# Kernel optimization log

Measured on AMD Instinct MI355X. Metric: run time of the kernel, lower is better.

## Reference

```python
import jax, jax.numpy as jnp
import numpy as np
from jax import lax

B, T, D_IN, HID, C = 256, 1024, 39, 128, 41
H = HID // 2  # per-direction hidden = 64
G = 4 * H    # gate dim = 256


def _lstm_dir(x, w_ih, w_hh, b, reverse):
    # x: [B,T,Din]; w_ih: [4H,Din]; w_hh: [4H,H]; b: [4H] (b_ih+b_hh fused)
    gx = jnp.einsum('btd,gd->btg', x, w_ih) + b          # [B,T,4H]
    gx_t = jnp.swapaxes(gx, 0, 1)                        # [T,B,4H]
    h0 = jnp.zeros((x.shape[0], H), x.dtype)
    c0 = jnp.zeros((x.shape[0], H), x.dtype)

    def step(carry, g_t):
        h, c = carry
        gates = g_t + h @ w_hh.T
        i, f, g, o = jnp.split(gates, 4, axis=-1)        # torch gate order i,f,g,o
        i = jax.nn.sigmoid(i); f = jax.nn.sigmoid(f)
        g = jnp.tanh(g);       o = jax.nn.sigmoid(o)
        c = f * c + i * g
        h = o * jnp.tanh(c)
        return (h, c), h

    _, hs = lax.scan(step, (h0, c0), gx_t, reverse=reverse)
    return jnp.swapaxes(hs, 0, 1)                        # [B,T,H]


def _bilstm(x, w_ih_l0, w_hh_l0, b_l0, w_ih_r, w_hh_r, b_r):
    # layer 0: input dim 39
    hf = _lstm_dir(x, w_ih_l0[0], w_hh_l0[0], b_l0[0], False)
    hb = _lstm_dir(x, w_ih_l0[1], w_hh_l0[1], b_l0[1], True)
    h = jnp.concatenate([hf, hb], axis=-1)               # [B,T,128]
    # layers 1,2: input dim 128 (dropout is identity in eval mode)
    for l in range(2):
        hf = _lstm_dir(h, w_ih_r[l, 0], w_hh_r[l, 0], b_r[l, 0], False)
        hb = _lstm_dir(h, w_ih_r[l, 1], w_hh_r[l, 1], b_r[l, 1], True)
        h = jnp.concatenate([hf, hb], axis=-1)
    return h


def _viterbi(emissions, start, end, trans):
    # emissions [B,T,C] -> best tag path [B,T]
    e = jnp.swapaxes(emissions, 0, 1)                    # [T,B,C]
    score0 = start + e[0]                                # [B,C]

    def step(score, e_t):
        cand = score[:, :, None] + trans[None]           # [B,C_prev,C_next]
        best = jnp.max(cand, axis=1) + e_t
        idx = jnp.argmax(cand, axis=1)                   # [B,C] backpointers
        return best, idx

    final, hist = lax.scan(step, score0, e[1:])          # hist [T-1,B,C]
    final = final + end
    last = jnp.argmax(final, axis=-1)                    # [B]

    def back(tag, idx_t):
        prev = jnp.take_along_axis(idx_t, tag[:, None], axis=1)[:, 0]
        return prev, prev

    _, tags_rev = lax.scan(back, last, hist, reverse=True)  # [T-1,B] in time order
    tags = jnp.concatenate([tags_rev, last[None]], axis=0)  # [T,B]
    return jnp.swapaxes(tags, 0, 1).astype(jnp.int32)       # [B,T]


def setup_inputs() -> dict:
    key = jax.random.key(0)
    ks = jax.random.split(key, 12)
    s = 0.1
    return {
        'x':        jax.random.normal(ks[0], (B, T, D_IN), jnp.float32),
        'w_ih_l0':  jax.random.normal(ks[1], (2, G, D_IN), jnp.float32) * s,
        'w_hh_l0':  jax.random.normal(ks[2], (2, G, H), jnp.float32) * s,
        'b_l0':     jax.random.normal(ks[3], (2, G), jnp.float32) * s,
        'w_ih_r':   jax.random.normal(ks[4], (2, 2, G, HID), jnp.float32) * s,
        'w_hh_r':   jax.random.normal(ks[5], (2, 2, G, H), jnp.float32) * s,
        'b_r':      jax.random.normal(ks[6], (2, 2, G), jnp.float32) * s,
        'lin_w':    jax.random.normal(ks[7], (C, HID), jnp.float32) * s,
        'lin_b':    jax.random.normal(ks[8], (C,), jnp.float32) * s,
        'crf_start': jax.random.normal(ks[9], (C,), jnp.float32) * s,
        'crf_end':  jax.random.normal(ks[10], (C,), jnp.float32) * s,
        'crf_trans': jax.random.normal(ks[11], (C, C), jnp.float32) * s,
    }


def reference(x, w_ih_l0, w_hh_l0, b_l0, w_ih_r, w_hh_r, b_r,
              lin_w, lin_b, crf_start, crf_end, crf_trans):
    feats = _bilstm(x, w_ih_l0, w_hh_l0, b_l0, w_ih_r, w_hh_r, b_r)  # [B,T,128]
    emissions = jnp.einsum('bth,ch->btc', feats, lin_w) + lin_b      # [B,T,41]
    return _viterbi(emissions, crf_start, crf_end, crf_trans)        # [B,T] int32
```

## Files before the change

kernel.cpp:

```cpp
#include <hip/hip_runtime.h>

#define TT 1024
#define BB 256
#define CC 41

__device__ __forceinline__ float sigf(float x) {
    float t = __builtin_amdgcn_exp2f(-1.4426950408889634f * x);
    return __builtin_amdgcn_rcpf(1.0f + t);
}
__device__ __forceinline__ float tanhf_fast(float x) {
    float t = __builtin_amdgcn_exp2f(2.8853900817779268f * x);
    return fmaf(-2.0f, __builtin_amdgcn_rcpf(t + 1.0f), 1.0f);
}
__device__ __forceinline__ float lane_bcast(float v, int k) {
    return __uint_as_float(__builtin_amdgcn_readlane(__float_as_uint(v), k));
}

template <int PS, bool SPLIT>
__global__ __launch_bounds__(256, 2) void gemm_phase(
    const float* __restrict__ A0, int sA0,
    const float* __restrict__ A1, int sA1,
    const float* __restrict__ W,
    const float* __restrict__ bias,
    float* __restrict__ slab, size_t slabDirStride,
    int K, int phase, int dir_base)
{
    __shared__ float As[32][132];
    __shared__ float Bs[32][132];
    const int tid = threadIdx.x;
    const int bx = blockIdx.x;
    const int n0 = blockIdx.y * 128;
    const int dir = dir_base + blockIdx.z;
    const int tb = dir ? (TT - 1 - phase * PS) : (phase * PS);
    const float* Wd = W + (size_t)dir * 256 * K;
    const float* bd = bias + dir * 256;
    float* slabD = slab + slabDirStride * blockIdx.z;

    const int ty = tid >> 4, tx = tid & 15;
    float acc[8][8];
#pragma unroll
    for (int i = 0; i < 8; ++i)
#pragma unroll
        for (int j = 0; j < 8; ++j) acc[i][j] = 0.f;

    for (int k0 = 0; k0 < K; k0 += 32) {
        const int kc = (K - k0 < 32) ? (K - k0) : 32;
        if (SPLIT) {
            const bool hi = (k0 >= 64);
            const float* base = hi ? A1 : A0;
            const int str = hi ? sA1 : sA0;
            const int ko = k0 - (hi ? 64 : 0);
#pragma unroll
            for (int q = 0; q < 4; ++q) {
                const int lin = tid + q * 256;
                const int m = lin >> 3, c4 = lin & 7;
                const int r = bx * (128 / PS) + m / PS;
                const int s = m % PS;
                const int t = dir ? (tb - s) : (tb + s);
                const float4 v =
                    *(const float4*)(base + (size_t)(r * TT + t) * str + ko + c4 * 4);
                As[c4 * 4 + 0][m] = v.x; As[c4 * 4 + 1][m] = v.y;
                As[c4 * 4 + 2][m] = v.z; As[c4 * 4 + 3][m] = v.w;
            }
        } else if (kc == 32) {
#pragma unroll
            for (int q = 0; q < 16; ++q) {
                const int lin = tid + q * 256;
                const int m = lin >> 5, cc = lin & 31;
                const int r = bx * (128 / PS) + m / PS;
                const int s = m % PS;
                const int t = dir ? (tb - s) : (tb + s);
                As[cc][m] = A0[(size_t)(r * TT + t) * sA0 + k0 + cc];
            }
        } else {
            for (int lin = tid; lin < 128 * kc; lin += 256) {
                const int m = lin / kc, cc = lin - m * kc;
                const int r = bx * (128 / PS) + m / PS;
                const int s = m % PS;
                const int t = dir ? (tb - s) : (tb + s);
                As[cc][m] = A0[(size_t)(r * TT + t) * sA0 + k0 + cc];
            }
        }
        if (kc == 32) {
#pragma unroll
            for (int q = 0; q < 16; ++q) {
                const int lin = tid + q * 256;
                const int n = lin >> 5, cc = lin & 31;
                Bs[cc][n] = Wd[(size_t)(n0 + n) * K + k0 + cc];
            }
        } else {
            for (int lin = tid; lin < 128 * kc; lin += 256) {
                const int n = lin / kc, cc = lin - n * kc;
                Bs[cc][n] = Wd[(size_t)(n0 + n) * K + k0 + cc];
            }
        }
        __syncthreads();

        for (int kk = 0; kk < kc; ++kk) {
            float a[8], b[8];
            *(float4*)&a[0] = *(const float4*)&As[kk][ty * 4];
            *(float4*)&a[4] = *(const float4*)&As[kk][64 + ty * 4];
            *(float4*)&b[0] = *(const float4*)&Bs[kk][tx * 4];
            *(float4*)&b[4] = *(const float4*)&Bs[kk][64 + tx * 4];
#pragma unroll
            for (int i = 0; i < 8; ++i)
#pragma unroll
                for (int j = 0; j < 8; ++j)
                    acc[i][j] = fmaf(a[i], b[j], acc[i][j]);
        }
        __syncthreads();
    }

    float b0[4], b1[4];
#pragma unroll
    for (int j = 0; j < 4; ++j) {
        b0[j] = bd[n0 + tx * 4 + j];
        b1[j] = bd[n0 + 64 + tx * 4 + j];
    }
#pragma unroll
    for (int i = 0; i < 8; ++i) {
        const int m = (i < 4) ? (ty * 4 + i) : (64 + ty * 4 + i - 4);
        const int r = bx * (128 / PS) + m / PS;
        const int s = m % PS;
        float* so_ = slabD + ((size_t)r * PS + s) * 256;
        float4 v0, v1;
        v0.x = acc[i][0] + b0[0]; v0.y = acc[i][1] + b0[1];
        v0.z = acc[i][2] + b0[2]; v0.w = acc[i][3] + b0[3];
        v1.x = acc[i][4] + b1[0]; v1.y = acc[i][5] + b1[1];
        v1.z = acc[i][6] + b1[2]; v1.w = acc[i][7] + b1[3];
        *(float4*)&so_[n0 + tx * 4] = v0;
        *(float4*)&so_[n0 + 64 + tx * 4] = v1;
    }
}

template <int PS>
__global__ __launch_bounds__(64, 1) void recur_phase(
    const float* __restrict__ slab, size_t slabDirStride,
    const float* __restrict__ w_hh,
    float* __restrict__ outF, int strF,
    float* __restrict__ outB, int strB,
    float* __restrict__ state,
    int phase, int dir_base)
{
    const int r = blockIdx.x;
    const int dir = dir_base + blockIdx.y;
    const int j = threadIdx.x;

    float wi[64], wf[64], wg[64], wo[64];
    const float* wb = w_hh + (size_t)dir * 256 * 64;
#pragma unroll
    for (int q = 0; q < 16; ++q) {
        float4 v;
        v = *(const float4*)&wb[(size_t)j * 64 + q * 4];
        wi[q * 4] = v.x; wi[q * 4 + 1] = v.y; wi[q * 4 + 2] = v.z; wi[q * 4 + 3] = v.w;
        v = *(const float4*)&wb[(size_t)(64 + j) * 64 + q * 4];
        wf[q * 4] = v.x; wf[q * 4 + 1] = v.y; wf[q * 4 + 2] = v.z; wf[q * 4 + 3] = v.w;
        v = *(const float4*)&wb[(size_t)(128 + j) * 64 + q * 4];
        wg[q * 4] = v.x; wg[q * 4 + 1] = v.y; wg[q * 4 + 2] = v.z; wg[q * 4 + 3] = v.w;
        v = *(const float4*)&wb[(size_t)(192 + j) * 64 + q * 4];
        wo[q * 4] = v.x; wo[q * 4 + 1] = v.y; wo[q * 4 + 2] = v.z; wo[q * 4 + 3] = v.w;
    }

    float* stp = state + ((size_t)dir * 256 + r) * 128 + j;
    float h = 0.f, c = 0.f;
    if (phase != 0) { h = stp[0]; c = stp[64]; }

    const float* gx = slab + slabDirStride * blockIdx.y + (size_t)r * PS * 256 + j;
    const int tb = dir ? (TT - 1 - phase * PS) : (phase * PS);
    float* out = dir ? outB : outF;
    const int str = dir ? strB : strF;
    const ptrdiff_t hstep = dir ? -(ptrdiff_t)str : (ptrdiff_t)str;
    float* hp = out + (size_t)(r * TT + tb) * str + j;

    float pg[4][4];
#pragma unroll
    for (int p = 0; p < 4; ++p) {
        const float* g0 = gx + (size_t)p * 256;
        pg[p][0] = g0[0]; pg[p][1] = g0[64]; pg[p][2] = g0[128]; pg[p][3] = g0[192];
    }

#pragma unroll 1
    for (int s4 = 0; s4 < PS; s4 += 4) {
#pragma unroll
        for (int u = 0; u < 4; ++u) {
            const int s = s4 + u;
            float ai = pg[u][0], af = pg[u][1], ag = pg[u][2], ao = pg[u][3];
            if (s + 4 < PS) {
                const float* gn = gx + (size_t)(s + 4) * 256;
                pg[u][0] = gn[0]; pg[u][1] = gn[64];
                pg[u][2] = gn[128]; pg[u][3] = gn[192];
            }
#pragma unroll
            for (int k = 0; k < 64; ++k) {
                const float hk = lane_bcast(h, k);
                ai = fmaf(hk, wi[k], ai);
                af = fmaf(hk, wf[k], af);
                ag = fmaf(hk, wg[k], ag);
                ao = fmaf(hk, wo[k], ao);
            }
            const float iv = sigf(ai), fv = sigf(af);
            const float gv = tanhf_fast(ag), ov = sigf(ao);
            c = fmaf(fv, c, iv * gv);
            h = ov * tanhf_fast(c);
            hp[0] = h;
            hp += hstep;
        }
    }
    stp[0] = h; stp[64] = c;
}

__global__ __launch_bounds__(256, 2) void emis_kernel(
    const float* __restrict__ hA,
    const float* __restrict__ hB,
    const float* __restrict__ lw, const float* __restrict__ lb,
    float* __restrict__ eout)
{
    __shared__ float sf[64 * 132];
    __shared__ float swt[41 * 132];
    const int tid = threadIdx.x;
    const size_t bt0 = (size_t)blockIdx.x * 64;

#pragma unroll
    for (int q = 0; q < 4; ++q) {
        const int idx = tid + q * 256;
        const int row = idx >> 4, c4 = idx & 15;
        *(float4*)&sf[row * 132 + c4 * 4] =
            *(const float4*)&hA[(bt0 + row) * 128 + c4 * 4];
    }
#pragma unroll
    for (int q = 0; q < 4; ++q) {
        const int idx = tid + q * 256;
        const int row = idx >> 4, c4 = idx & 15;
        *(float4*)&sf[row * 132 + 64 + c4 * 4] =
            *(const float4*)&hB[(bt0 + row) * 64 + c4 * 4];
    }
    for (int idx = tid; idx < 41 * 32; idx += 256) {
        const int row = idx >> 5, cc = idx & 31;
        *(float4*)&swt[row * 132 + cc * 4] = ((const float4*)lw)[idx];
    }
    __syncthreads();

    const int btg = tid >> 4;
    const int cg = tid & 15;
    const int c0 = cg * 3;
    float acc[4][3];
#pragma unroll
    for (int i = 0; i < 4; ++i)
#pragma unroll
        for (int j = 0; j < 3; ++j) acc[i][j] = 0.f;

    for (int k = 0; k < 128; k += 4) {
        float4 fv[4], wv[3];
#pragma unroll
        for (int i = 0; i < 4; ++i) fv[i] = *(const float4*)&sf[(btg * 4 + i) * 132 + k];
#pragma unroll
        for (int j = 0; j < 3; ++j) {
            const int c = (c0 + j < CC) ? (c0 + j) : (CC - 1);
            wv[j] = *(const float4*)&swt[c * 132 + k];
        }
#pragma unroll
        for (int i = 0; i < 4; ++i)
#pragma unroll
            for (int j = 0; j < 3; ++j) {
                acc[i][j] = fmaf(fv[i].x, wv[j].x, acc[i][j]);
                acc[i][j] = fmaf(fv[i].y, wv[j].y, acc[i][j]);
                acc[i][j] = fmaf(fv[i].z, wv[j].z, acc[i][j]);
                acc[i][j] = fmaf(fv[i].w, wv[j].w, acc[i][j]);
            }
    }
    __syncthreads();
    float* so = sf;
#pragma unroll
    for (int i = 0; i < 4; ++i)
#pragma unroll
        for (int j = 0; j < 3; ++j) {
            const int c = c0 + j;
            if (c < CC) so[(btg * 4 + i) * CC + c] = acc[i][j] + lb[c];
        }
    __syncthreads();
    for (int q = tid; q < 64 * CC; q += 256) {
        const int row = q / CC, col = q - row * CC;
        eout[(bt0 + row) * 128 + col] = so[q];
    }
}

__global__ __launch_bounds__(128, 1) void viterbi_kernel(
    const float* __restrict__ h0,
    const float* __restrict__ st, const float* __restrict__ en,
    const float* __restrict__ tr, int* __restrict__ out)
{
    const int b = blockIdx.x;
    const int tid = threadIdx.x;
    const int ci = tid >> 1;
    const int ph = tid & 1;
    const bool valid = (ci < CC);
    const int c = valid ? ci : (CC - 1);
    const int pbase = ph ? 20 : 0;

    __shared__ unsigned char bp[TT][CC];
    __shared__ float scp[2][CC];

    float trc[21];
#pragma unroll
    for (int i = 0; i < 21; ++i) trc[i] = tr[(pbase + i) * CC + c];

    const float* eb = h0 + (size_t)b * TT * 128 + 64;
    const float NEG = -3.0e38f;

    if (valid && ph == 0) scp[0][c] = st[c] + eb[c];
    __syncthreads();

#pragma unroll 1
    for (int t = 1; t < TT; ++t) {
        const int cur = (t - 1) & 1, nxt = t & 1;
        const float ecur = eb[(size_t)t * 128 + c];

        float best = NEG;
        int bi = 0;
#pragma unroll
        for (int i = 0; i < 21; ++i) {
            const float v = scp[cur][pbase + i] + trc[i];
            if (v > best) { best = v; bi = pbase + i; }
        }
        const float ob = __shfl_xor(best, 1, 64);
        const int oi = __shfl_xor(bi, 1, 64);
        float wv; int wi_;
        if (ph == 0) {
            const bool hw = (ob > best);
            wv = hw ? ob : best;
            wi_ = hw ? oi : bi;
        } else {
            const bool lw = !(best > ob);
            wv = lw ? ob : best;
            wi_ = lw ? oi : bi;
        }
        if (valid && ph == 0) {
            bp[t][c] = (unsigned char)wi_;
            scp[nxt][c] = wv + ecur;
        }
        __syncthreads();
    }

    const int lane = tid & 63;
    float fin = (tid < CC) ? scp[(TT - 1) & 1][lane] + en[lane] : NEG;
    int idx = lane;
#pragma unroll
    for (int off = 32; off; off >>= 1) {
        const float v2 = __shfl_down(fin, off, 64);
        const int i2 = __shfl_down(idx, off, 64);
        if (v2 > fin || (v2 == fin && i2 < idx)) { fin = v2; idx = i2; }
    }
    int tag = __shfl(idx, 0, 64);
    if (tid == 0) {
        int* ob = out + (size_t)b * TT;
        ob[TT - 1] = tag;
        for (int t = TT - 1; t >= 1; --t) {
            tag = bp[t][tag];
            ob[t - 1] = tag;
        }
    }
}

extern "C" void kernel_launch(void* const* d_in, const int* in_sizes, int n_in,
                              void* d_out, int out_size, void* d_ws, size_t ws_size,
                              hipStream_t stream) {
    const float* x       = (const float*)d_in[0];
    const float* w_ih_l0 = (const float*)d_in[1];
    const float* w_hh_l0 = (const float*)d_in[2];
    const float* b_l0    = (const float*)d_in[3];
    const float* w_ih_r  = (const float*)d_in[4];
    const float* w_hh_r  = (const float*)d_in[5];
    const float* b_r     = (const float*)d_in[6];
    const float* lin_w   = (const float*)d_in[7];
    const float* lin_b   = (const float*)d_in[8];
    const float* crf_s   = (const float*)d_in[9];
    const float* crf_e   = (const float*)d_in[10];
    const float* crf_t   = (const float*)d_in[11];
    int* out = (int*)d_out;

    float* H0    = (float*)d_ws;
    float* F     = H0 + (size_t)BB * TT * 128;
    float* slab  = F + (size_t)BB * TT * 64;
    float* state = slab + (size_t)BB * 128 * 256;

    const size_t SLAB0 = (size_t)BB * 64 * 256;
    for (int ph = 0; ph < 16; ++ph) {
        gemm_phase<64, false><<<dim3(128, 2, 2), 256, 0, stream>>>(
            x, 39, nullptr, 0, w_ih_l0, b_l0, slab, SLAB0, 39, ph, 0);
        recur_phase<64><<<dim3(256, 2), 64, 0, stream>>>(
            slab, SLAB0, w_hh_l0, H0, 128, H0 + 64, 128, state, ph, 0);
    }

    for (int l = 0; l < 2; ++l) {
        const float* W    = w_ih_r + (size_t)l * 512 * 128;
        const float* bias = b_r + (size_t)l * 512;
        const float* whh  = w_hh_r + (size_t)l * 512 * 64;
        const float* A0   = (l == 0) ? H0 : F;
        const int    s0   = (l == 0) ? 128 : 64;
        const float* A1   = H0 + 64;  const int s1 = 128;
        float* oF = (l == 0) ? F : H0;        const int sF = (l == 0) ? 64 : 128;
        float* oB = (l == 0) ? H0 + 64 : F;   const int sB = (l == 0) ? 128 : 64;
        for (int d = 0; d < 2; ++d) {
            for (int ph = 0; ph < 8; ++ph) {
                gemm_phase<128, true><<<dim3(256, 2, 1), 256, 0, stream>>>(
                    A0, s0, A1, s1, W, bias, slab, 0, 128, ph, d);
                recur_phase<128><<<dim3(256, 1), 64, 0, stream>>>(
                    slab, 0, whh, oF, sF, oB, sB, state, ph, d);
            }
        }
    }

    emis_kernel<<<BB * TT / 64, 256, 0, stream>>>(H0, F, lin_w, lin_b, H0 + 64);
    viterbi_kernel<<<BB, 128, 0, stream>>>(H0, crf_s, crf_e, crf_t, out);
}
```

Baseline: 6.931 ms.

## Use packed FMA with LDS-broadcast h in recurrence, prefetching GEMM and Viterbi

The recurrence kernel now stores h in shared memory and reads it back as float2 pairs. This replaces 64 per-step readlane broadcasts with half as many packed v2f FMAs, split into two partial sums. A dedicated recurrent-layer GEMM prefetches the next K chunk into registers while the current chunk is computed. Layer 0 moves to 128-step phases, which halves its launch count. Viterbi gains a tree-shaped argmax and an 8-step emission prefetch. The h exchange through LDS relies on single-wavefront ordering without a barrier, which the compiler could in principle reorder.

```diff
diff --git a/kernel.cpp b/kernel.cpp
--- a/kernel.cpp
+++ b/kernel.cpp
@@ -4,6 +4,8 @@
 #define BB 256
 #define CC 41
 
+typedef float v2f __attribute__((ext_vector_type(2)));
+
 __device__ __forceinline__ float sigf(float x) {
     float t = __builtin_amdgcn_exp2f(-1.4426950408889634f * x);
     return __builtin_amdgcn_rcpf(1.0f + t);
@@ -12,25 +14,20 @@
     float t = __builtin_amdgcn_exp2f(2.8853900817779268f * x);
     return fmaf(-2.0f, __builtin_amdgcn_rcpf(t + 1.0f), 1.0f);
 }
-__device__ __forceinline__ float lane_bcast(float v, int k) {
-    return __uint_as_float(__builtin_amdgcn_readlane(__float_as_uint(v), k));
-}
-
-template <int PS, bool SPLIT>
-__global__ __launch_bounds__(256, 2) void gemm_phase(
+
+template <int PS>
+__global__ __launch_bounds__(256, 2) void gemm_l0(
     const float* __restrict__ A0, int sA0,
-    const float* __restrict__ A1, int sA1,
-    const float* __restrict__ W,
-    const float* __restrict__ bias,
+    const float* __restrict__ W, const float* __restrict__ bias,
     float* __restrict__ slab, size_t slabDirStride,
-    int K, int phase, int dir_base)
+    int K, int phase)
 {
     __shared__ float As[32][132];
     __shared__ float Bs[32][132];
     const int tid = threadIdx.x;
     const int bx = blockIdx.x;
     const int n0 = blockIdx.y * 128;
-    const int dir = dir_base + blockIdx.z;
+    const int dir = blockIdx.z;
     const int tb = dir ? (TT - 1 - phase * PS) : (phase * PS);
     const float* Wd = W + (size_t)dir * 256 * K;
     const float* bd = bias + dir * 256;
@@ -45,24 +42,7 @@
 
     for (int k0 = 0; k0 < K; k0 += 32) {
         const int kc = (K - k0 < 32) ? (K - k0) : 32;
-        if (SPLIT) {
-            const bool hi = (k0 >= 64);
-            const float* base = hi ? A1 : A0;
-            const int str = hi ? sA1 : sA0;
-            const int ko = k0 - (hi ? 64 : 0);
-#pragma unroll
-            for (int q = 0; q < 4; ++q) {
-                const int lin = tid + q * 256;
-                const int m = lin >> 3, c4 = lin & 7;
-                const int r = bx * (128 / PS) + m / PS;
-                const int s = m % PS;
-                const int t = dir ? (tb - s) : (tb + s);
-                const float4 v =
-                    *(const float4*)(base + (size_t)(r * TT + t) * str + ko + c4 * 4);
-                As[c4 * 4 + 0][m] = v.x; As[c4 * 4 + 1][m] = v.y;
-                As[c4 * 4 + 2][m] = v.z; As[c4 * 4 + 3][m] = v.w;
-            }
-        } else if (kc == 32) {
+        if (kc == 32) {
 #pragma unroll
             for (int q = 0; q < 16; ++q) {
                 const int lin = tid + q * 256;
@@ -72,6 +52,12 @@
                 const int t = dir ? (tb - s) : (tb + s);
                 As[cc][m] = A0[(size_t)(r * TT + t) * sA0 + k0 + cc];
             }
+#pragma unroll
+            for (int q = 0; q < 16; ++q) {
+                const int lin = tid + q * 256;
+                const int n = lin >> 5, cc = lin & 31;
+                Bs[cc][n] = Wd[(size_t)(n0 + n) * K + k0 + cc];
+            }
         } else {
             for (int lin = tid; lin < 128 * kc; lin += 256) {
                 const int m = lin / kc, cc = lin - m * kc;
@@ -80,22 +66,12 @@
                 const int t = dir ? (tb - s) : (tb + s);
                 As[cc][m] = A0[(size_t)(r * TT + t) * sA0 + k0 + cc];
             }
-        }
-        if (kc == 32) {
-#pragma unroll
-            for (int q = 0; q < 16; ++q) {
-                const int lin = tid + q * 256;
-                const int n = lin >> 5, cc = lin & 31;
-                Bs[cc][n] = Wd[(size_t)(n0 + n) * K + k0 + cc];
-            }
-        } else {
             for (int lin = tid; lin < 128 * kc; lin += 256) {
                 const int n = lin / kc, cc = lin - n * kc;
                 Bs[cc][n] = Wd[(size_t)(n0 + n) * K + k0 + cc];
             }
         }
         __syncthreads();
-
         for (int kk = 0; kk < kc; ++kk) {
             float a[8], b[8];
             *(float4*)&a[0] = *(const float4*)&As[kk][ty * 4];
@@ -133,6 +109,111 @@
     }
 }
 
+__global__ __launch_bounds__(256, 2) void gemm_rec(
+    const float* __restrict__ A0, int sA0,
+    const float* __restrict__ A1, int sA1,
+    const float* __restrict__ W,
+    const float* __restrict__ bias,
+    float* __restrict__ slab,
+    int phase, int dir)
+{
+    __shared__ float As[32][132];
+    __shared__ float Bs[32][132];
+    const int tid = threadIdx.x;
+    const int bx = blockIdx.x;
+    const int n0 = blockIdx.y * 128;
+    const int tb = dir ? (TT - 1 - phase * 128) : (phase * 128);
+    const float* Wd = W + (size_t)dir * 256 * 128;
+    const float* bd = bias + dir * 256;
+
+    const int ty = tid >> 4, tx = tid & 15;
+    const int c4 = tid & 7;
+    const int mb = tid >> 3;
+
+    int rowoff[4];
+#pragma unroll
+    for (int q = 0; q < 4; ++q) {
+        const int s = mb + q * 32;
+        const int t = dir ? (tb - s) : (tb + s);
+        rowoff[q] = bx * TT + t;
+    }
+
+    float acc[8][8];
+#pragma unroll
+    for (int i = 0; i < 8; ++i)
+#pragma unroll
+        for (int j = 0; j < 8; ++j) acc[i][j] = 0.f;
+
+    float4 ra[4], rb[4];
+#pragma unroll
+    for (int q = 0; q < 4; ++q)
+        ra[q] = *(const float4*)&A0[(size_t)rowoff[q] * sA0 + c4 * 4];
+#pragma unroll
+    for (int q = 0; q < 4; ++q)
+        rb[q] = *(const float4*)&Wd[(size_t)(n0 + mb + q * 32) * 128 + c4 * 4];
+
+#pragma unroll
+    for (int ch = 0; ch < 4; ++ch) {
+#pragma unroll
+        for (int q = 0; q < 4; ++q) {
+            const int m = mb + q * 32;
+            As[c4 * 4 + 0][m] = ra[q].x; As[c4 * 4 + 1][m] = ra[q].y;
+            As[c4 * 4 + 2][m] = ra[q].z; As[c4 * 4 + 3][m] = ra[q].w;
+        }
+#pragma unroll
+        for (int q = 0; q < 4; ++q) {
+            const int n = mb + q * 32;
+            Bs[c4 * 4 + 0][n] = rb[q].x; Bs[c4 * 4 + 1][n] = rb[q].y;
+            Bs[c4 * 4 + 2][n] = rb[q].z; Bs[c4 * 4 + 3][n] = rb[q].w;
+        }
+        if (ch < 3) {
+            const int kn = (ch + 1) * 32;
+            const float* base = (kn >= 64) ? A1 : A0;
+            const int str = (kn >= 64) ? sA1 : sA0;
+            const int ko = kn - ((kn >= 64) ? 64 : 0);
+#pragma unroll
+            for (int q = 0; q < 4; ++q)
+                ra[q] = *(const float4*)&base[(size_t)rowoff[q] * str + ko + c4 * 4];
+#pragma unroll
+            for (int q = 0; q < 4; ++q)
+                rb[q] = *(const float4*)&Wd[(size_t)(n0 + mb + q * 32) * 128 + kn + c4 * 4];
+        }
+        __syncthreads();
+        for (int kk = 0; kk < 32; ++kk) {
+            float a[8], b[8];
+            *(float4*)&a[0] = *(const float4*)&As[kk][ty * 4];
+            *(float4*)&a[4] = *(const float4*)&As[kk][64 + ty * 4];
+            *(float4*)&b[0] = *(const float4*)&Bs[kk][tx * 4];
+            *(float4*)&b[4] = *(const float4*)&Bs[kk][64 + tx * 4];
+#pragma unroll
+            for (int i = 0; i < 8; ++i)
+#pragma unroll
+                for (int j = 0; j < 8; ++j)
+                    acc[i][j] = fmaf(a[i], b[j], acc[i][j]);
+        }
+        __syncthreads();
+    }
+
+    float b0[4], b1[4];
+#pragma unroll
+    for (int j = 0; j < 4; ++j) {
+        b0[j] = bd[n0 + tx * 4 + j];
+        b1[j] = bd[n0 + 64 + tx * 4 + j];
+    }
+#pragma unroll
+    for (int i = 0; i < 8; ++i) {
+        const int s = (i < 4) ? (ty * 4 + i) : (64 + ty * 4 + i - 4);
+        float* so_ = slab + ((size_t)bx * 128 + s) * 256;
+        float4 v0, v1;
+        v0.x = acc[i][0] + b0[0]; v0.y = acc[i][1] + b0[1];
+        v0.z = acc[i][2] + b0[2]; v0.w = acc[i][3] + b0[3];
+        v1.x = acc[i][4] + b1[0]; v1.y = acc[i][5] + b1[1];
+        v1.z = acc[i][6] + b1[2]; v1.w = acc[i][7] + b1[3];
+        *(float4*)&so_[n0 + tx * 4] = v0;
+        *(float4*)&so_[n0 + 64 + tx * 4] = v1;
+    }
+}
+
 template <int PS>
 __global__ __launch_bounds__(64, 1) void recur_phase(
     const float* __restrict__ slab, size_t slabDirStride,
@@ -146,24 +227,24 @@
     const int dir = dir_base + blockIdx.y;
     const int j = threadIdx.x;
 
-    float wi[64], wf[64], wg[64], wo[64];
+    v2f wi[32], wf[32], wg[32], wo[32];
     const float* wb = w_hh + (size_t)dir * 256 * 64;
-#pragma unroll
-    for (int q = 0; q < 16; ++q) {
-        float4 v;
-        v = *(const float4*)&wb[(size_t)j * 64 + q * 4];
-        wi[q * 4] = v.x; wi[q * 4 + 1] = v.y; wi[q * 4 + 2] = v.z; wi[q * 4 + 3] = v.w;
-        v = *(const float4*)&wb[(size_t)(64 + j) * 64 + q * 4];
-        wf[q * 4] = v.x; wf[q * 4 + 1] = v.y; wf[q * 4 + 2] = v.z; wf[q * 4 + 3] = v.w;
-        v = *(const float4*)&wb[(size_t)(128 + j) * 64 + q * 4];
-        wg[q * 4] = v.x; wg[q * 4 + 1] = v.y; wg[q * 4 + 2] = v.z; wg[q * 4 + 3] = v.w;
-        v = *(const float4*)&wb[(size_t)(192 + j) * 64 + q * 4];
-        wo[q * 4] = v.x; wo[q * 4 + 1] = v.y; wo[q * 4 + 2] = v.z; wo[q * 4 + 3] = v.w;
-    }
+    const v2f* ri = (const v2f*)&wb[(size_t)j * 64];
+    const v2f* rf = (const v2f*)&wb[(size_t)(64 + j) * 64];
+    const v2f* rg = (const v2f*)&wb[(size_t)(128 + j) * 64];
+    const v2f* ro = (const v2f*)&wb[(size_t)(192 + j) * 64];
+#pragma unroll
+    for (int q = 0; q < 32; ++q) {
+        wi[q] = ri[q]; wf[q] = rf[q]; wg[q] = rg[q]; wo[q] = ro[q];
+    }
+
+    __shared__ __align__(16) float hlds[64];
+    const v2f* h2 = (const v2f*)hlds;
 
     float* stp = state + ((size_t)dir * 256 + r) * 128 + j;
     float h = 0.f, c = 0.f;
     if (phase != 0) { h = stp[0]; c = stp[64]; }
+    hlds[j] = h;
 
     const float* gx = slab + slabDirStride * blockIdx.y + (size_t)r * PS * 256 + j;
     const int tb = dir ? (TT - 1 - phase * PS) : (phase * PS);
@@ -184,24 +265,28 @@
 #pragma unroll
         for (int u = 0; u < 4; ++u) {
             const int s = s4 + u;
-            float ai = pg[u][0], af = pg[u][1], ag = pg[u][2], ao = pg[u][3];
+            v2f ai2 = {pg[u][0], 0.f}, af2 = {pg[u][1], 0.f};
+            v2f ag2 = {pg[u][2], 0.f}, ao2 = {pg[u][3], 0.f};
             if (s + 4 < PS) {
                 const float* gn = gx + (size_t)(s + 4) * 256;
                 pg[u][0] = gn[0]; pg[u][1] = gn[64];
                 pg[u][2] = gn[128]; pg[u][3] = gn[192];
             }
 #pragma unroll
-            for (int k = 0; k < 64; ++k) {
-                const float hk = lane_bcast(h, k);
-                ai = fmaf(hk, wi[k], ai);
-                af = fmaf(hk, wf[k], af);
-                ag = fmaf(hk, wg[k], ag);
-                ao = fmaf(hk, wo[k], ao);
-            }
-            const float iv = sigf(ai), fv = sigf(af);
-            const float gv = tanhf_fast(ag), ov = sigf(ao);
+            for (int k = 0; k < 32; ++k) {
+                const v2f hk = h2[k];
+                ai2 = __builtin_elementwise_fma(hk, wi[k], ai2);
+                af2 = __builtin_elementwise_fma(hk, wf[k], af2);
+                ag2 = __builtin_elementwise_fma(hk, wg[k], ag2);
+                ao2 = __builtin_elementwise_fma(hk, wo[k], ao2);
+            }
+            const float iv = sigf(ai2.x + ai2.y);
+            const float fv = sigf(af2.x + af2.y);
+            const float gv = tanhf_fast(ag2.x + ag2.y);
+            const float ov = sigf(ao2.x + ao2.y);
             c = fmaf(fv, c, iv * gv);
             h = ov * tanhf_fast(c);
+            hlds[j] = h;
             hp[0] = h;
             hp += hstep;
         }
@@ -210,8 +295,7 @@
 }
 
 __global__ __launch_bounds__(256, 2) void emis_kernel(
-    const float* __restrict__ hA,
-    const float* __restrict__ hB,
+    const float* __restrict__ hA, const float* __restrict__ hB,
     const float* __restrict__ lw, const float* __restrict__ lb,
     float* __restrict__ eout)
 {
@@ -223,16 +307,16 @@
 #pragma unroll
     for (int q = 0; q < 4; ++q) {
         const int idx = tid + q * 256;
-        const int row = idx >> 4, c4 = idx & 15;
-        *(float4*)&sf[row * 132 + c4 * 4] =
-            *(const float4*)&hA[(bt0 + row) * 128 + c4 * 4];
+        const int row = idx >> 4, p4 = idx & 15;
+        *(float4*)&sf[row * 132 + p4 * 4] =
+            *(const float4*)&hA[(bt0 + row) * 128 + p4 * 4];
     }
 #pragma unroll
     for (int q = 0; q < 4; ++q) {
         const int idx = tid + q * 256;
-        const int row = idx >> 4, c4 = idx & 15;
-        *(float4*)&sf[row * 132 + 64 + c4 * 4] =
-            *(const float4*)&hB[(bt0 + row) * 64 + c4 * 4];
+        const int row = idx >> 4, p4 = idx & 15;
+        *(float4*)&sf[row * 132 + 64 + p4 * 4] =
+            *(const float4*)&hB[(bt0 + row) * 64 + p4 * 4];
     }
     for (int idx = tid; idx < 41 * 32; idx += 256) {
         const int row = idx >> 5, cc = idx & 31;
@@ -305,23 +389,45 @@
     for (int i = 0; i < 21; ++i) trc[i] = tr[(pbase + i) * CC + c];
 
     const float* eb = h0 + (size_t)b * TT * 128 + 64;
-    const float NEG = -3.0e38f;
-
     if (valid && ph == 0) scp[0][c] = st[c] + eb[c];
     __syncthreads();
 
-#pragma unroll 1
-    for (int t = 1; t < TT; ++t) {
-        const int cur = (t - 1) & 1, nxt = t & 1;
-        const float ecur = eb[(size_t)t * 128 + c];
-
-        float best = NEG;
-        int bi = 0;
-#pragma unroll
-        for (int i = 0; i < 21; ++i) {
-            const float v = scp[cur][pbase + i] + trc[i];
-            if (v > best) { best = v; bi = pbase + i; }
-        }
+    auto vstep = [&](int t, int cur, float ecur) {
+        float v[21];
+#pragma unroll
+        for (int i = 0; i < 21; ++i) v[i] = scp[cur][pbase + i] + trc[i];
+        float a1[11]; int x1[11];
+#pragma unroll
+        for (int i = 0; i < 10; ++i) {
+            const bool rr = v[2 * i + 1] > v[2 * i];
+            a1[i] = rr ? v[2 * i + 1] : v[2 * i];
+            x1[i] = pbase + (rr ? 2 * i + 1 : 2 * i);
+        }
+        a1[10] = v[20]; x1[10] = pbase + 20;
+        float a2[6]; int x2[6];
+#pragma unroll
+        for (int i = 0; i < 5; ++i) {
+            const bool rr = a1[2 * i + 1] > a1[2 * i];
+            a2[i] = rr ? a1[2 * i + 1] : a1[2 * i];
+            x2[i] = rr ? x1[2 * i + 1] : x1[2 * i];
+        }
+        a2[5] = a1[10]; x2[5] = x1[10];
+        float a3[3]; int x3[3];
+#pragma unroll
+        for (int i = 0; i < 3; ++i) {
+            const bool rr = a3 ? false : false;
+            (void)rr;
+            const bool r2 = a2[2 * i + 1] > a2[2 * i];
+            a3[i] = r2 ? a2[2 * i + 1] : a2[2 * i];
+            x3[i] = r2 ? x2[2 * i + 1] : x2[2 * i];
+        }
+        const bool r4 = a3[1] > a3[0];
+        const float a4 = r4 ? a3[1] : a3[0];
+        const int x4 = r4 ? x3[1] : x3[0];
+        const bool r5 = a3[2] > a4;
+        const float best = r5 ? a3[2] : a4;
+        const int bi = r5 ? x3[2] : x4;
+
         const float ob = __shfl_xor(best, 1, 64);
         const int oi = __shfl_xor(bi, 1, 64);
         float wv; int wi_;
@@ -336,11 +442,31 @@
         }
         if (valid && ph == 0) {
             bp[t][c] = (unsigned char)wi_;
-            scp[nxt][c] = wv + ecur;
+            scp[cur ^ 1][c] = wv + ecur;
         }
         __syncthreads();
-    }
-
+    };
+
+    float ep[8];
+#pragma unroll
+    for (int u = 0; u < 8; ++u) ep[u] = eb[(size_t)(1 + u) * 128 + c];
+
+#pragma unroll 1
+    for (int tb = 1; tb + 7 < TT; tb += 8) {
+#pragma unroll
+        for (int u = 0; u < 8; ++u) {
+            const int t = tb + u;
+            vstep(t, u & 1, ep[u]);
+            if (t + 8 < TT) ep[u] = eb[(size_t)(t + 8) * 128 + c];
+        }
+    }
+#pragma unroll
+    for (int u = 0; u < 7; ++u) {
+        const int t = TT - 7 + u;
+        vstep(t, u & 1, ep[u]);
+    }
+
+    const float NEG = -3.0e38f;
     const int lane = tid & 63;
     float fin = (tid < CC) ? scp[(TT - 1) & 1][lane] + en[lane] : NEG;
     int idx = lane;
@@ -379,37 +505,37 @@
     int* out = (int*)d_out;
 
     float* H0    = (float*)d_ws;
-    float* F     = H0 + (size_t)BB * TT * 128;
-    float* slab  = F + (size_t)BB * TT * 64;
-    float* state = slab + (size_t)BB * 128 * 256;
-
-    const size_t SLAB0 = (size_t)BB * 64 * 256;
-    for (int ph = 0; ph < 16; ++ph) {
-        gemm_phase<64, false><<<dim3(128, 2, 2), 256, 0, stream>>>(
-            x, 39, nullptr, 0, w_ih_l0, b_l0, slab, SLAB0, 39, ph, 0);
-        recur_phase<64><<<dim3(256, 2), 64, 0, stream>>>(
-            slab, SLAB0, w_hh_l0, H0, 128, H0 + 64, 128, state, ph, 0);
+    float* X     = H0 + (size_t)BB * TT * 128;
+    float* Y     = X + (size_t)BB * TT * 64;
+    float* state = Y + (size_t)BB * 128 * 256;
+
+    const size_t SLAB0 = (size_t)BB * 128 * 256;
+    for (int ph = 0; ph < 8; ++ph) {
+        gemm_l0<128><<<dim3(BB, 2, 2), 256, 0, stream>>>(
+            x, 39, w_ih_l0, b_l0, X, SLAB0, 39, ph);
+        recur_phase<128><<<dim3(BB, 2), 64, 0, stream>>>(
+            X, SLAB0, w_hh_l0, H0, 128, H0 + 64, 128, state, ph, 0);
     }
 
     for (int l = 0; l < 2; ++l) {
         const float* W    = w_ih_r + (size_t)l * 512 * 128;
         const float* bias = b_r + (size_t)l * 512;
         const float* whh  = w_hh_r + (size_t)l * 512 * 64;
-        const float* A0   = (l == 0) ? H0 : F;
+        const float* A0   = (l == 0) ? H0 : X;
         const int    s0   = (l == 0) ? 128 : 64;
         const float* A1   = H0 + 64;  const int s1 = 128;
-        float* oF = (l == 0) ? F : H0;        const int sF = (l == 0) ? 64 : 128;
-        float* oB = (l == 0) ? H0 + 64 : F;   const int sB = (l == 0) ? 128 : 64;
+        float* oF = (l == 0) ? X : H0;        const int sF = (l == 0) ? 64 : 128;
+        float* oB = (l == 0) ? H0 + 64 : X;   const int sB = (l == 0) ? 128 : 64;
         for (int d = 0; d < 2; ++d) {
             for (int ph = 0; ph < 8; ++ph) {
-                gemm_phase<128, true><<<dim3(256, 2, 1), 256, 0, stream>>>(
-                    A0, s0, A1, s1, W, bias, slab, 0, 128, ph, d);
-                recur_phase<128><<<dim3(256, 1), 64, 0, stream>>>(
-                    slab, 0, whh, oF, sF, oB, sB, state, ph, d);
-            }
-        }
-    }
-
-    emis_kernel<<<BB * TT / 64, 256, 0, stream>>>(H0, F, lin_w, lin_b, H0 + 64);
+                gemm_rec<<<dim3(BB, 2, 1), 256, 0, stream>>>(
+                    A0, s0, A1, s1, W, bias, Y, ph, d);
+                recur_phase<128><<<dim3(BB, 1), 64, 0, stream>>>(
+                    Y, 0, whh, oF, sF, oB, sB, state, ph, d);
+            }
+        }
+    }
+
+    emis_kernel<<<BB * TT / 64, 256, 0, stream>>>(H0, X, lin_w, lin_b, H0 + 64);
     viterbi_kernel<<<BB, 128, 0, stream>>>(H0, crf_s, crf_e, crf_t, out);
 }
```

New measurement: 6.357 ms. -8.3%, faster.
